# Kernel optimization log

Hardware: AMD Instinct MI355X
Metric: run time of the kernel (lower is better)

## Reference

```python
import jax, jax.numpy as jnp
import numpy as np

N_NODES = 100000
N_EDGES = 1600000
IN_DIM = 128
HID = 128
NUM_LAYERS = 10
NUM_CLASSES = 2
NUM_GRAPHS = 64


def setup_inputs() -> dict:
    key = jax.random.key(0)
    ks = jax.random.split(key, 16)
    x = jax.random.normal(ks[0], (N_NODES, IN_DIM), dtype=jnp.float32)
    # edges with no self loops (GIN_Conv calls remove_self_loops)
    src = jax.random.randint(ks[1], (N_EDGES,), 0, N_NODES)
    off = jax.random.randint(ks[2], (N_EDGES,), 1, N_NODES)
    dst = (src + off) % N_NODES
    edge_index = jnp.stack([src, dst]).astype(jnp.int64)
    batch = jnp.sort(jax.random.randint(ks[3], (N_NODES,), 0, NUM_GRAPHS)).astype(jnp.int64)
    s = 1.0 / np.sqrt(HID)
    eps = jnp.zeros((NUM_LAYERS,), dtype=jnp.float32)
    W1 = jax.random.normal(ks[4], (NUM_LAYERS, IN_DIM, HID), dtype=jnp.float32) * s
    b1 = jnp.zeros((NUM_LAYERS, HID), dtype=jnp.float32)
    W2 = jax.random.normal(ks[5], (NUM_LAYERS, HID, HID), dtype=jnp.float32) * s
    b2 = jnp.zeros((NUM_LAYERS, HID), dtype=jnp.float32)
    Wc1 = jax.random.normal(ks[6], (HID, HID), dtype=jnp.float32) * s
    bc1 = jnp.zeros((HID,), dtype=jnp.float32)
    Wc2 = jax.random.normal(ks[7], (HID, NUM_CLASSES), dtype=jnp.float32) * s
    bc2 = jnp.zeros((NUM_CLASSES,), dtype=jnp.float32)
    return {"x": x, "edge_index": edge_index, "batch": batch, "eps": eps,
            "W1": W1, "b1": b1, "W2": W2, "b2": b2,
            "Wc1": Wc1, "bc1": bc1, "Wc2": Wc2, "bc2": bc2}


def _gin_block(x, src, dst, eps_i, W1_i, b1_i, W2_i, b2_i, mlp_residual):
    # gather-scatter add aggregation: aggr[v] = sum_{(u->v)} x[u]
    aggr = jax.ops.segment_sum(x[src], dst, num_segments=N_NODES)
    h = (1.0 + eps_i) * x + aggr
    out = jnp.dot(jax.nn.relu(jnp.dot(h, W1_i) + b1_i), W2_i) + b2_i
    if mlp_residual:  # MLP internal residual (layers i > 0)
        out = out + h
    out = jax.nn.relu(out)  # ResidualGNNBlock: Identity norm, relu, Identity dropout
    out = out + x  # block residual (dims match: in_dim == hidden)
    return out


def reference(x, edge_index, batch, eps, W1, b1, W2, b2, Wc1, bc1, Wc2, bc2):
    src, dst = edge_index[0], edge_index[1]
    for i in range(NUM_LAYERS):
        x = _gin_block(x, src, dst, eps[i], W1[i], b1[i], W2[i], b2[i], mlp_residual=(i > 0))
    # global_mean_pool
    sums = jax.ops.segment_sum(x, batch, num_segments=NUM_GRAPHS)
    cnts = jax.ops.segment_sum(jnp.ones((x.shape[0], 1), x.dtype), batch, num_segments=NUM_GRAPHS)
    pooled = sums / jnp.maximum(cnts, 1.0)
    # classifier MLP (dropout inactive in eval)
    logits = jnp.dot(jax.nn.relu(jnp.dot(pooled, Wc1) + bc1), Wc2) + bc2
    return logits
```

## Files before the change

kernel.cpp:

```cpp
#include <hip/hip_runtime.h>

#define N_NODES 100000
#define N_EDGES 1600000
#define HID 128
#define NUM_LAYERS 10
#define NUM_GRAPHS 64
#define SCAN_BLOCKS ((N_NODES + 255) / 256)
#define IDX_CAP 2048


__global__ __launch_bounds__(256) void count_deg_kernel(const int* __restrict__ dst,
                                                        int* __restrict__ deg, int E) {
  int e = blockIdx.x * 256 + threadIdx.x;
  if (e < E) atomicAdd(&deg[dst[e]], 1);
}

__global__ __launch_bounds__(256) void block_sum_kernel(const int* __restrict__ deg,
                                                        int* __restrict__ psum, int n) {
  __shared__ int sd[256];
  int i = blockIdx.x * 256 + threadIdx.x;
  sd[threadIdx.x] = (i < n) ? deg[i] : 0;
  __syncthreads();
  for (int off = 128; off > 0; off >>= 1) {
    if (threadIdx.x < off) sd[threadIdx.x] += sd[threadIdx.x + off];
    __syncthreads();
  }
  if (threadIdx.x == 0) psum[blockIdx.x] = sd[0];
}

__global__ __launch_bounds__(512) void scan_partials_kernel(const int* __restrict__ psum,
                                                            int* __restrict__ poff, int nb) {
  __shared__ int sd[512];
  int i = threadIdx.x;
  int v = (i < nb) ? psum[i] : 0;
  sd[i] = v;
  __syncthreads();
  for (int off = 1; off < 512; off <<= 1) {
    int t = (i >= off) ? sd[i - off] : 0;
    __syncthreads();
    sd[i] += t;
    __syncthreads();
  }
  if (i < nb) poff[i] = sd[i] - v;
}

__global__ __launch_bounds__(256) void write_rs_kernel(const int* __restrict__ deg,
                                                       const int* __restrict__ poff,
                                                       int* __restrict__ rs,
                                                       int* __restrict__ cur, int n) {
  __shared__ int sd[256];
  int i = blockIdx.x * 256 + threadIdx.x;
  int v = (i < n) ? deg[i] : 0;
  sd[threadIdx.x] = v;
  __syncthreads();
  for (int off = 1; off < 256; off <<= 1) {
    int t = (threadIdx.x >= off) ? sd[threadIdx.x - off] : 0;
    __syncthreads();
    sd[threadIdx.x] += t;
    __syncthreads();
  }
  if (i < n) {
    int incl = poff[blockIdx.x] + sd[threadIdx.x];
    rs[i + 1] = incl;
    cur[i] = incl - v;
  }
  if (i == 0) rs[0] = 0;
}

__global__ __launch_bounds__(256) void fill_csr_kernel(const int* __restrict__ src,
                                                       const int* __restrict__ dst,
                                                       int* __restrict__ cur,
                                                       int* __restrict__ csr, int E) {
  int e = blockIdx.x * 256 + threadIdx.x;
  if (e < E) {
    int p = atomicAdd(&cur[dst[e]], 1);
    csr[p] = src[e];
  }
}


__global__ __launch_bounds__(256, 3) void layer_kernel(const float* __restrict__ xin,
                                                       float* __restrict__ xout,
                                                       const int* __restrict__ rs,
                                                       const int* __restrict__ csr,
                                                       const float* __restrict__ eps, int layer,
                                                       const float* __restrict__ W1,
                                                       const float* __restrict__ b1,
                                                       const float* __restrict__ W2,
                                                       const float* __restrict__ b2,
                                                       int n, int addH) {
  __shared__ float lh[64 * 128];
  __shared__ int lidx[IDX_CAP];
  __shared__ int lrs[65];
  const int tid = threadIdx.x;
  const int row0 = blockIdx.x * 64;
  const float4* x4 = (const float4*)xin;
  float4* lh4 = (float4*)lh;
  const float s = 1.0f + eps[layer];

  int rowEnd = row0 + 64; if (rowEnd > n) rowEnd = n;
  const int eBase = rs[row0];
  const int cnt = rs[rowEnd] - eBase;
  if (tid < 65) {
    int node = row0 + tid; if (node > n) node = n;
    lrs[tid] = rs[node] - eBase;
  }
  const int stage = (cnt < IDX_CAP) ? cnt : IDX_CAP;
  for (int t = tid; t < stage; t += 256) lidx[t] = csr[eBase + t];
  __syncthreads();

  const int w = tid >> 5;
  const int lane = tid & 31;
  const int base8 = 8 * w;

  {
    float4 sv[8];
#pragma unroll
    for (int r = 0; r < 8; ++r) {
      int node = row0 + base8 + r;
      if (node < n) sv[r] = x4[node * 32 + lane];
    }
#pragma unroll
    for (int r = 0; r < 8; ++r) {
      int node = row0 + base8 + r;
      float4 o; o.x = o.y = o.z = o.w = 0.f;
      if (node < n) { o.x = sv[r].x * s; o.y = sv[r].y * s; o.z = sv[r].z * s; o.w = sv[r].w * s; }
      lh4[(base8 + r) * 32 + lane] = o;
    }
  }

  if (cnt <= IDX_CAP) {
    int eLo = lrs[base8];
    int eHi = lrs[base8 + 8];
    int cn = base8;
    int ce = lrs[base8 + 1];
    int c = eLo;
    float4 acc; acc.x = acc.y = acc.z = acc.w = 0.f;

#define FLUSH_WHILE()                                                      \
    while (c >= ce) {                                                      \
      float4 _t = lh4[cn * 32 + lane];                                     \
      _t.x += acc.x; _t.y += acc.y; _t.z += acc.z; _t.w += acc.w;          \
      lh4[cn * 32 + lane] = _t;                                            \
      acc.x = acc.y = acc.z = acc.w = 0.f;                                 \
      ++cn; ce = lrs[cn + 1];                                              \
    }
#define CONS(B)                                                            \
    { FLUSH_WHILE();                                                       \
      acc.x += (B).x; acc.y += (B).y; acc.z += (B).z; acc.w += (B).w;      \
      ++c; }

    const int np = eHi - eLo;
    if (np >= 8) {
      float4 b0 = x4[lidx[eLo + 0] * 32 + lane];
      float4 b1v = x4[lidx[eLo + 1] * 32 + lane];
      float4 b2v = x4[lidx[eLo + 2] * 32 + lane];
      float4 b3 = x4[lidx[eLo + 3] * 32 + lane];
      float4 b4 = x4[lidx[eLo + 4] * 32 + lane];
      float4 b5 = x4[lidx[eLo + 5] * 32 + lane];
      float4 b6 = x4[lidx[eLo + 6] * 32 + lane];
      float4 b7 = x4[lidx[eLo + 7] * 32 + lane];
      int issue = eLo + 8;
      while (issue + 8 <= eHi) {
        CONS(b0); b0 = x4[lidx[issue + 0] * 32 + lane];
        CONS(b1v); b1v = x4[lidx[issue + 1] * 32 + lane];
        CONS(b2v); b2v = x4[lidx[issue + 2] * 32 + lane];
        CONS(b3); b3 = x4[lidx[issue + 3] * 32 + lane];
        CONS(b4); b4 = x4[lidx[issue + 4] * 32 + lane];
        CONS(b5); b5 = x4[lidx[issue + 5] * 32 + lane];
        CONS(b6); b6 = x4[lidx[issue + 6] * 32 + lane];
        CONS(b7); b7 = x4[lidx[issue + 7] * 32 + lane];
        issue += 8;
      }
      const int rem = eHi - issue;
      float4 r0, r1, r2, r3, r4, r5, r6;
      if (rem > 0) r0 = x4[lidx[issue + 0] * 32 + lane];
      if (rem > 1) r1 = x4[lidx[issue + 1] * 32 + lane];
      if (rem > 2) r2 = x4[lidx[issue + 2] * 32 + lane];
      if (rem > 3) r3 = x4[lidx[issue + 3] * 32 + lane];
      if (rem > 4) r4 = x4[lidx[issue + 4] * 32 + lane];
      if (rem > 5) r5 = x4[lidx[issue + 5] * 32 + lane];
      if (rem > 6) r6 = x4[lidx[issue + 6] * 32 + lane];
      CONS(b0); CONS(b1v); CONS(b2v); CONS(b3);
      CONS(b4); CONS(b5); CONS(b6); CONS(b7);
      if (rem > 0) CONS(r0);
      if (rem > 1) CONS(r1);
      if (rem > 2) CONS(r2);
      if (rem > 3) CONS(r3);
      if (rem > 4) CONS(r4);
      if (rem > 5) CONS(r5);
      if (rem > 6) CONS(r6);
    } else if (np > 0) {
      float4 r0, r1, r2, r3, r4, r5, r6;
      if (np > 0) r0 = x4[lidx[eLo + 0] * 32 + lane];
      if (np > 1) r1 = x4[lidx[eLo + 1] * 32 + lane];
      if (np > 2) r2 = x4[lidx[eLo + 2] * 32 + lane];
      if (np > 3) r3 = x4[lidx[eLo + 3] * 32 + lane];
      if (np > 4) r4 = x4[lidx[eLo + 4] * 32 + lane];
      if (np > 5) r5 = x4[lidx[eLo + 5] * 32 + lane];
      if (np > 6) r6 = x4[lidx[eLo + 6] * 32 + lane];
      if (np > 0) CONS(r0);
      if (np > 1) CONS(r1);
      if (np > 2) CONS(r2);
      if (np > 3) CONS(r3);
      if (np > 4) CONS(r4);
      if (np > 5) CONS(r5);
      if (np > 6) CONS(r6);
    }
    {
      float4 t = lh4[cn * 32 + lane];
      t.x += acc.x; t.y += acc.y; t.z += acc.z; t.w += acc.w;
      lh4[cn * 32 + lane] = t;
    }
#undef CONS
#undef FLUSH_WHILE
  } else {
#pragma unroll
    for (int r = 0; r < 8; ++r) {
      int node = row0 + base8 + r;
      if (node >= n) continue;
      float4 t = lh4[(base8 + r) * 32 + lane];
      int e0 = rs[node], e1 = rs[node + 1];
      for (int e = e0; e < e1; ++e) {
        int u = csr[e];
        float4 v = x4[u * 32 + lane];
        t.x += v.x; t.y += v.y; t.z += v.z; t.w += v.w;
      }
      lh4[(base8 + r) * 32 + lane] = t;
    }
  }
  __syncthreads();

  const int cg = tid & 31;
  const int rg = tid >> 5;
  float acc[8][4];
#pragma unroll
  for (int r = 0; r < 8; ++r) { acc[r][0] = acc[r][1] = acc[r][2] = acc[r][3] = 0.f; }

  for (int k4 = 0; k4 < 32; ++k4) {
    float4 w0 = *(const float4*)(W1 + (k4 * 4 + 0) * 128 + cg * 4);
    float4 w1 = *(const float4*)(W1 + (k4 * 4 + 1) * 128 + cg * 4);
    float4 w2 = *(const float4*)(W1 + (k4 * 4 + 2) * 128 + cg * 4);
    float4 w3 = *(const float4*)(W1 + (k4 * 4 + 3) * 128 + cg * 4);
#pragma unroll
    for (int r = 0; r < 8; ++r) {
      float4 a = *(const float4*)(lh + (rg * 8 + r) * 128 + k4 * 4);
      acc[r][0] += a.x * w0.x + a.y * w1.x + a.z * w2.x + a.w * w3.x;
      acc[r][1] += a.x * w0.y + a.y * w1.y + a.z * w2.y + a.w * w3.y;
      acc[r][2] += a.x * w0.z + a.y * w1.z + a.z * w2.z + a.w * w3.z;
      acc[r][3] += a.x * w0.w + a.y * w1.w + a.z * w2.w + a.w * w3.w;
    }
  }

  float4 hreg[8];
#pragma unroll
  for (int r = 0; r < 8; ++r) hreg[r] = *(const float4*)(lh + (rg * 8 + r) * 128 + cg * 4);
  __syncthreads();

  {
    float4 bb = *(const float4*)(b1 + cg * 4);
#pragma unroll
    for (int r = 0; r < 8; ++r) {
      float4 o;
      o.x = fmaxf(acc[r][0] + bb.x, 0.f);
      o.y = fmaxf(acc[r][1] + bb.y, 0.f);
      o.z = fmaxf(acc[r][2] + bb.z, 0.f);
      o.w = fmaxf(acc[r][3] + bb.w, 0.f);
      *(float4*)(lh + (rg * 8 + r) * 128 + cg * 4) = o;
      acc[r][0] = acc[r][1] = acc[r][2] = acc[r][3] = 0.f;
    }
  }
  __syncthreads();

  for (int k4 = 0; k4 < 32; ++k4) {
    float4 w0 = *(const float4*)(W2 + (k4 * 4 + 0) * 128 + cg * 4);
    float4 w1 = *(const float4*)(W2 + (k4 * 4 + 1) * 128 + cg * 4);
    float4 w2 = *(const float4*)(W2 + (k4 * 4 + 2) * 128 + cg * 4);
    float4 w3 = *(const float4*)(W2 + (k4 * 4 + 3) * 128 + cg * 4);
#pragma unroll
    for (int r = 0; r < 8; ++r) {
      float4 a = *(const float4*)(lh + (rg * 8 + r) * 128 + k4 * 4);
      acc[r][0] += a.x * w0.x + a.y * w1.x + a.z * w2.x + a.w * w3.x;
      acc[r][1] += a.x * w0.y + a.y * w1.y + a.z * w2.y + a.w * w3.y;
      acc[r][2] += a.x * w0.z + a.y * w1.z + a.z * w2.z + a.w * w3.z;
      acc[r][3] += a.x * w0.w + a.y * w1.w + a.z * w2.w + a.w * w3.w;
    }
  }

  float4 b2v = *(const float4*)(b2 + cg * 4);
  float4* xo4 = (float4*)xout;
#pragma unroll
  for (int r = 0; r < 8; ++r) {
    int row = row0 + rg * 8 + r;
    if (row < n) {
      float ox = acc[r][0] + b2v.x;
      float oy = acc[r][1] + b2v.y;
      float oz = acc[r][2] + b2v.z;
      float ow = acc[r][3] + b2v.w;
      if (addH) {
        ox += hreg[r].x; oy += hreg[r].y; oz += hreg[r].z; ow += hreg[r].w;
      }
      ox = fmaxf(ox, 0.f); oy = fmaxf(oy, 0.f); oz = fmaxf(oz, 0.f); ow = fmaxf(ow, 0.f);
      float4 xv = x4[row * 32 + cg];
      float4 o;
      o.x = ox + xv.x; o.y = oy + xv.y; o.z = oz + xv.z; o.w = ow + xv.w;
      xo4[row * 32 + cg] = o;
    }
  }
}


__global__ __launch_bounds__(128) void pool_kernel(const float* __restrict__ x,
                                                   const int* __restrict__ batch,
                                                   float* __restrict__ pool,
                                                   int* __restrict__ gcnt, int n) {
  const int CH = 512;
  int c = threadIdx.x;
  int n0 = blockIdx.x * CH;
  if (n0 >= n) return;
  int n1 = n0 + CH; if (n1 > n) n1 = n;
  float acc = 0.f;
  int g = batch[n0];
  int cl = 0;
  for (int i = n0; i < n1; ++i) {
    int gi = batch[i];
    if (gi != g) {
      atomicAdd(&pool[g * 128 + c], acc);
      if (c == 0) atomicAdd(&gcnt[g], cl);
      acc = 0.f; cl = 0; g = gi;
    }
    acc += x[i * 128 + c];
    cl++;
  }
  atomicAdd(&pool[g * 128 + c], acc);
  if (c == 0) atomicAdd(&gcnt[g], cl);
}


__global__ __launch_bounds__(128) void classifier_kernel(const float* __restrict__ pool,
                                                         const int* __restrict__ gcnt,
                                                         const float* __restrict__ Wc1,
                                                         const float* __restrict__ bc1,
                                                         const float* __restrict__ Wc2,
                                                         const float* __restrict__ bc2,
                                                         float* __restrict__ out) {
  __shared__ float prow[128];
  __shared__ float hid[128];
  int g = blockIdx.x;
  int c = threadIdx.x;
  float cf = (float)gcnt[g];
  if (cf < 1.f) cf = 1.f;
  prow[c] = pool[g * 128 + c] / cf;
  __syncthreads();
  float a = bc1[c];
  for (int k = 0; k < 128; ++k) a += prow[k] * Wc1[k * 128 + c];
  hid[c] = fmaxf(a, 0.f);
  __syncthreads();
  if (c < 2) {
    float a2 = bc2[c];
    for (int k = 0; k < 128; ++k) a2 += hid[k] * Wc2[k * 2 + c];
    out[g * 2 + c] = a2;
  }
}


extern "C" void kernel_launch(void* const* d_in, const int* in_sizes, int n_in,
                              void* d_out, int out_size, void* d_ws, size_t ws_size,
                              hipStream_t stream) {
  const float* x_in = (const float*)d_in[0];
  const int* edge_index = (const int*)d_in[1];
  const int* batch = (const int*)d_in[2];
  const float* eps = (const float*)d_in[3];
  const float* W1 = (const float*)d_in[4];
  const float* b1 = (const float*)d_in[5];
  const float* W2 = (const float*)d_in[6];
  const float* b2 = (const float*)d_in[7];
  const float* Wc1 = (const float*)d_in[8];
  const float* bc1 = (const float*)d_in[9];
  const float* Wc2 = (const float*)d_in[10];
  const float* bc2 = (const float*)d_in[11];
  float* out = (float*)d_out;

  const int N = N_NODES, E = N_EDGES;
  const int* src = edge_index;
  const int* dst = edge_index + E;

  float* xa = (float*)d_ws;
  float* xb = xa + (size_t)N * 128;
  int* deg = (int*)(xb + (size_t)N * 128);
  int* rs = deg + N;
  int* cur = rs + (N + 1);
  int* csr = cur + N;
  float* pool = (float*)(csr + E);
  int* gcnt = (int*)(pool + NUM_GRAPHS * 128);
  int* psum = gcnt + NUM_GRAPHS;
  int* poff = psum + SCAN_BLOCKS;

  hipMemsetAsync(deg, 0, N * sizeof(int), stream);

  count_deg_kernel<<<(E + 255) / 256, 256, 0, stream>>>(dst, deg, E);
  block_sum_kernel<<<SCAN_BLOCKS, 256, 0, stream>>>(deg, psum, N);
  scan_partials_kernel<<<1, 512, 0, stream>>>(psum, poff, SCAN_BLOCKS);
  write_rs_kernel<<<SCAN_BLOCKS, 256, 0, stream>>>(deg, poff, rs, cur, N);
  fill_csr_kernel<<<(E + 255) / 256, 256, 0, stream>>>(src, dst, cur, csr, E);

  for (int i = 0; i < NUM_LAYERS; ++i) {
    const float* xi = (i == 0) ? x_in : ((i % 2 == 0) ? xb : xa);
    float* xo = (i % 2 == 0) ? xa : xb;
    layer_kernel<<<(N + 63) / 64, 256, 0, stream>>>(xi, xo, rs, csr, eps, i,
                                                    W1 + (size_t)i * 128 * 128, b1 + (size_t)i * 128,
                                                    W2 + (size_t)i * 128 * 128, b2 + (size_t)i * 128,
                                                    N, i > 0 ? 1 : 0);
  }
  const float* xfin = (NUM_LAYERS % 2 == 0) ? xb : xa;

  hipMemsetAsync(pool, 0, NUM_GRAPHS * 128 * sizeof(float), stream);
  hipMemsetAsync(gcnt, 0, NUM_GRAPHS * sizeof(int), stream);
  pool_kernel<<<(N + 511) / 512, 128, 0, stream>>>(xfin, batch, pool, gcnt, N);
  classifier_kernel<<<NUM_GRAPHS, 128, 0, stream>>>(pool, gcnt, Wc1, bc1, Wc2, bc2, out);
}
```

Baseline: 2.556 ms.

## Raise layer kernel occupancy, drop intra-block barriers, reuse input rows from registers

Shrinks the staged edge-index buffer so four blocks fit per CU instead of three, and raises the launch-bounds occupancy hint to match. Removes the block-wide barriers between aggregation and the two MLP GEMMs, since each 32-lane group only reads rows it wrote itself. The residual input rows stay in registers instead of being reloaded from global memory, and the MLP residual seeds the second GEMM's accumulator. The smaller index buffer sends slightly more tiles to the slower uncached fallback path. Keeping the input rows live across both GEMMs adds register pressure, which could cause spills at the higher occupancy target.

Measured after the change: 2.611 ms. 2.2% more time.

```diff
diff --git a/kernel.cpp b/kernel.cpp
--- a/kernel.cpp
+++ b/kernel.cpp
@@ -6,7 +6,8 @@
 #define NUM_LAYERS 10
 #define NUM_GRAPHS 64
 #define SCAN_BLOCKS ((N_NODES + 255) / 256)
-#define IDX_CAP 2048
+#define TILE 64
+#define IDX_CAP 1792
 
 
 __global__ __launch_bounds__(256) void count_deg_kernel(const int* __restrict__ dst,
@@ -79,7 +80,7 @@
 }
 
 
-__global__ __launch_bounds__(256, 3) void layer_kernel(const float* __restrict__ xin,
+__global__ __launch_bounds__(256, 4) void layer_kernel(const float* __restrict__ xin,
                                                        float* __restrict__ xout,
                                                        const int* __restrict__ rs,
                                                        const int* __restrict__ csr,
@@ -89,19 +90,19 @@
                                                        const float* __restrict__ W2,
                                                        const float* __restrict__ b2,
                                                        int n, int addH) {
-  __shared__ float lh[64 * 128];
+  __shared__ float lh[TILE * 128];
   __shared__ int lidx[IDX_CAP];
-  __shared__ int lrs[65];
+  __shared__ int lrs[TILE + 1];
   const int tid = threadIdx.x;
-  const int row0 = blockIdx.x * 64;
+  const int row0 = blockIdx.x * TILE;
   const float4* x4 = (const float4*)xin;
   float4* lh4 = (float4*)lh;
   const float s = 1.0f + eps[layer];
 
-  int rowEnd = row0 + 64; if (rowEnd > n) rowEnd = n;
+  int rowEnd = row0 + TILE; if (rowEnd > n) rowEnd = n;
   const int eBase = rs[row0];
   const int cnt = rs[rowEnd] - eBase;
-  if (tid < 65) {
+  if (tid < TILE + 1) {
     int node = row0 + tid; if (node > n) node = n;
     lrs[tid] = rs[node] - eBase;
   }
@@ -113,20 +114,18 @@
   const int lane = tid & 31;
   const int base8 = 8 * w;
 
-  {
-    float4 sv[8];
-#pragma unroll
-    for (int r = 0; r < 8; ++r) {
-      int node = row0 + base8 + r;
-      if (node < n) sv[r] = x4[node * 32 + lane];
-    }
-#pragma unroll
-    for (int r = 0; r < 8; ++r) {
-      int node = row0 + base8 + r;
-      float4 o; o.x = o.y = o.z = o.w = 0.f;
-      if (node < n) { o.x = sv[r].x * s; o.y = sv[r].y * s; o.z = sv[r].z * s; o.w = sv[r].w * s; }
-      lh4[(base8 + r) * 32 + lane] = o;
-    }
+  float4 sv[8];
+#pragma unroll
+  for (int r = 0; r < 8; ++r) {
+    int node = row0 + base8 + r;
+    if (node < n) sv[r] = x4[node * 32 + lane];
+    else { sv[r].x = sv[r].y = sv[r].z = sv[r].w = 0.f; }
+  }
+#pragma unroll
+  for (int r = 0; r < 8; ++r) {
+    float4 o;
+    o.x = sv[r].x * s; o.y = sv[r].y * s; o.z = sv[r].z * s; o.w = sv[r].w * s;
+    lh4[(base8 + r) * 32 + lane] = o;
   }
 
   if (cnt <= IDX_CAP) {
@@ -229,10 +228,9 @@
       lh4[(base8 + r) * 32 + lane] = t;
     }
   }
-  __syncthreads();
-
-  const int cg = tid & 31;
-  const int rg = tid >> 5;
+
+  const int cg = lane;
+  const int rg = w;
   float acc[8][4];
 #pragma unroll
   for (int r = 0; r < 8; ++r) { acc[r][0] = acc[r][1] = acc[r][2] = acc[r][3] = 0.f; }
@@ -252,25 +250,21 @@
     }
   }
 
-  float4 hreg[8];
-#pragma unroll
-  for (int r = 0; r < 8; ++r) hreg[r] = *(const float4*)(lh + (rg * 8 + r) * 128 + cg * 4);
-  __syncthreads();
-
   {
     float4 bb = *(const float4*)(b1 + cg * 4);
 #pragma unroll
     for (int r = 0; r < 8; ++r) {
+      float4 hv = *(const float4*)(lh + (rg * 8 + r) * 128 + cg * 4);
       float4 o;
       o.x = fmaxf(acc[r][0] + bb.x, 0.f);
       o.y = fmaxf(acc[r][1] + bb.y, 0.f);
       o.z = fmaxf(acc[r][2] + bb.z, 0.f);
       o.w = fmaxf(acc[r][3] + bb.w, 0.f);
       *(float4*)(lh + (rg * 8 + r) * 128 + cg * 4) = o;
-      acc[r][0] = acc[r][1] = acc[r][2] = acc[r][3] = 0.f;
-    }
-  }
-  __syncthreads();
+      if (addH) { acc[r][0] = hv.x; acc[r][1] = hv.y; acc[r][2] = hv.z; acc[r][3] = hv.w; }
+      else { acc[r][0] = acc[r][1] = acc[r][2] = acc[r][3] = 0.f; }
+    }
+  }
 
   for (int k4 = 0; k4 < 32; ++k4) {
     float4 w0 = *(const float4*)(W2 + (k4 * 4 + 0) * 128 + cg * 4);
@@ -293,17 +287,11 @@
   for (int r = 0; r < 8; ++r) {
     int row = row0 + rg * 8 + r;
     if (row < n) {
-      float ox = acc[r][0] + b2v.x;
-      float oy = acc[r][1] + b2v.y;
-      float oz = acc[r][2] + b2v.z;
-      float ow = acc[r][3] + b2v.w;
-      if (addH) {
-        ox += hreg[r].x; oy += hreg[r].y; oz += hreg[r].z; ow += hreg[r].w;
-      }
-      ox = fmaxf(ox, 0.f); oy = fmaxf(oy, 0.f); oz = fmaxf(oz, 0.f); ow = fmaxf(ow, 0.f);
-      float4 xv = x4[row * 32 + cg];
-      float4 o;
-      o.x = ox + xv.x; o.y = oy + xv.y; o.z = oz + xv.z; o.w = ow + xv.w;
+      float ox = fmaxf(acc[r][0] + b2v.x, 0.f) + sv[r].x;
+      float oy = fmaxf(acc[r][1] + b2v.y, 0.f) + sv[r].y;
+      float oz = fmaxf(acc[r][2] + b2v.z, 0.f) + sv[r].z;
+      float ow = fmaxf(acc[r][3] + b2v.w, 0.f) + sv[r].w;
+      float4 o; o.x = ox; o.y = oy; o.z = oz; o.w = ow;
       xo4[row * 32 + cg] = o;
     }
   }
@@ -407,7 +395,7 @@
   for (int i = 0; i < NUM_LAYERS; ++i) {
     const float* xi = (i == 0) ? x_in : ((i % 2 == 0) ? xb : xa);
     float* xo = (i % 2 == 0) ? xa : xb;
-    layer_kernel<<<(N + 63) / 64, 256, 0, stream>>>(xi, xo, rs, csr, eps, i,
+    layer_kernel<<<(N + TILE - 1) / TILE, 256, 0, stream>>>(xi, xo, rs, csr, eps, i,
                                                     W1 + (size_t)i * 128 * 128, b1 + (size_t)i * 128,
                                                     W2 + (size_t)i * 128 * 128, b2 + (size_t)i * 128,
                                                     N, i > 0 ? 1 : 0);
```
